# Optimization experiments

Hardware: AMD Instinct MI355X
Metric: run time of the kernel (lower is better)

The kernel has to match this reference:

```python
import jax, jax.numpy as jnp
import numpy as np

N_NODES = 50000
N_EDGES = 800000
D = 128          # embed_dim
H = 8            # heads
C = D // H       # per-head channels
F = 512          # ff_hidden_dim
LN_EPS = 1e-5
NEG_SLOPE = 0.2  # PyG GATConv default negative_slope


def _layernorm(x, g, b):
    mu = jnp.mean(x, axis=-1, keepdims=True)
    var = jnp.mean(jnp.square(x - mu), axis=-1, keepdims=True)
    return (x - mu) * jax.lax.rsqrt(var + LN_EPS) * g + b


def _gat_conv(x, edge_index, W, att_src, att_dst, bias):
    # PyG GATConv (concat=True, add_self_loops=True, shared lin for src/dst)
    N = x.shape[0]
    xl = (x @ W.T).reshape(N, H, C)                 # [N,H,C]
    a_s = jnp.sum(xl * att_src, axis=-1)            # [N,H]
    a_d = jnp.sum(xl * att_dst, axis=-1)            # [N,H]
    loops = jnp.arange(N)
    src = jnp.concatenate([edge_index[0], loops])   # [E+N]
    dst = jnp.concatenate([edge_index[1], loops])
    e = jax.nn.leaky_relu(a_s[src] + a_d[dst], NEG_SLOPE)  # [E+N,H]
    # segment softmax over incoming edges per destination node
    m = jax.ops.segment_max(e, dst, num_segments=N)
    m = jnp.where(jnp.isfinite(m), m, jnp.zeros_like(m))
    ex = jnp.exp(e - m[dst])
    s = jax.ops.segment_sum(ex, dst, num_segments=N)
    alpha = ex / (s[dst] + 1e-16)                   # [E+N,H]
    msg = xl[src] * alpha[:, :, None]               # [E+N,H,C]
    out = jax.ops.segment_sum(msg, dst, num_segments=N)  # [N,H,C]
    return out.reshape(N, H * C) + bias


def setup_inputs() -> dict:
    key = jax.random.key(0)
    ks = jax.random.split(key, 12)
    sc_d = 1.0 / np.sqrt(D)
    sc_f = 1.0 / np.sqrt(F)
    return {
        "x": jax.random.normal(ks[0], (N_NODES, D), dtype=jnp.float32),
        "virtual_edge_index": jax.random.randint(ks[1], (2, N_EDGES), 0, N_NODES, dtype=jnp.int64),
        "W_gat": jax.random.normal(ks[2], (H * C, D), dtype=jnp.float32) * sc_d,
        "att_src": jax.random.normal(ks[3], (H, C), dtype=jnp.float32) * sc_d,
        "att_dst": jax.random.normal(ks[4], (H, C), dtype=jnp.float32) * sc_d,
        "bias_gat": jnp.zeros((H * C,), dtype=jnp.float32),
        "W1": jax.random.normal(ks[5], (F, D), dtype=jnp.float32) * sc_d,
        "b1": jnp.zeros((F,), dtype=jnp.float32),
        "W2": jax.random.normal(ks[6], (D, F), dtype=jnp.float32) * sc_f,
        "b2": jnp.zeros((D,), dtype=jnp.float32),
        "g1": jnp.ones((D,), dtype=jnp.float32),
        "beta1": jnp.zeros((D,), dtype=jnp.float32),
        "g2": jnp.ones((D,), dtype=jnp.float32),
        "beta2": jnp.zeros((D,), dtype=jnp.float32),
    }


def reference(x, virtual_edge_index, W_gat, att_src, att_dst, bias_gat,
              W1, b1, W2, b2, g1, beta1, g2, beta2):
    h_gat = _gat_conv(x, virtual_edge_index, W_gat, att_src, att_dst, bias_gat)
    h = _layernorm(x + h_gat, g1, beta1)
    h_ff = jax.nn.relu(h @ W1.T + b1) @ W2.T + b2
    return _layernorm(h + h_ff, g2, beta2)
```

## Files before the change

kernel.cpp:

```cpp
#include <hip/hip_runtime.h>
#include <hip/hip_bf16.h>

#define N_NODES 50000
#define N_EDGES 800000
#define N_TOT   850000
#define DIM 128
#define HEADS 8
#define CH 16
#define FF 512
#define LN_EPS 1e-5f
#define NEG_SLOPE 0.2f

#define PART    8
#define NCHUNK  128
#define CHUNK_E (N_EDGES / NCHUNK)
#define NPP     (N_NODES / PART)
#define NHIST   (PART * NCHUNK)
#define NTILE   196

typedef __bf16 bf16x8 __attribute__((ext_vector_type(8)));
typedef float f32x4 __attribute__((ext_vector_type(4)));

__device__ __forceinline__ float bfr2f(unsigned short u) {
  return __uint_as_float(((unsigned)u) << 16);
}
__device__ __forceinline__ unsigned short f2bfr(float f) {
  __hip_bfloat16 h = __float2bfloat16(f);
  return *(unsigned short*)&h;
}
__device__ __forceinline__ float bf2f(__hip_bfloat16 h) { return __bfloat162float(h); }
__device__ __forceinline__ __hip_bfloat16 f2bf(float f) { return __float2bfloat16(f); }

__device__ __forceinline__ bf16x8 ldcvt8(const float* __restrict__ p) {
  const float4 a = ((const float4*)p)[0];
  const float4 b = ((const float4*)p)[1];
  bf16x8 r;
  r[0] = (__bf16)a.x; r[1] = (__bf16)a.y; r[2] = (__bf16)a.z; r[3] = (__bf16)a.w;
  r[4] = (__bf16)b.x; r[5] = (__bf16)b.y; r[6] = (__bf16)b.z; r[7] = (__bf16)b.w;
  return r;
}

__device__ __forceinline__ int ld_src(const int* ei, int mode, int e) {
  int v = mode ? ei[2 * e] : ei[e];
  return min(max(v, 0), N_NODES - 1);
}
__device__ __forceinline__ int ld_dst(const int* ei, int mode, int e) {
  int v = mode ? ei[2 * (N_EDGES + e)] : ei[N_EDGES + e];
  return min(max(v, 0), N_NODES - 1);
}
__device__ __forceinline__ int edge_mode(const int* __restrict__ ei) {
  int any = 0;
  for (int k = 1; k < 64; k += 2) any |= ei[k];
  return (any == 0) ? 1 : 0;
}

__device__ __forceinline__ float expleaky(float v) {
  v = v > 0.f ? v : NEG_SLOPE * v;
  return __expf(v);
}

__global__ __launch_bounds__(256) void k_xl(const float* __restrict__ x,
                                            const float* __restrict__ Wg,
                                            const float* __restrict__ att_s,
                                            const float* __restrict__ att_d,
                                            __hip_bfloat16* __restrict__ xl,
                                            float* __restrict__ a_s,
                                            float* __restrict__ a_d) {
  int gid = blockIdx.x * 256 + threadIdx.x;
  int w = gid >> 6;
  if (w >= 3125 * 2) return;
  int l = threadIdx.x & 63, quad = l >> 4, r = l & 15;
  int strip = w >> 1, cc = w & 1;
  f32x4 acc[4];
#pragma unroll
  for (int t = 0; t < 4; ++t) acc[t] = (f32x4){0.f, 0.f, 0.f, 0.f};
  int arow = strip * 16 + r;
  bf16x8 af[4];
#pragma unroll
  for (int kk = 0; kk < 4; ++kk) af[kk] = ldcvt8(x + arow * DIM + kk * 32 + quad * 8);
#pragma unroll
  for (int kk = 0; kk < 4; ++kk) {
    bf16x8 bfr[4];
#pragma unroll
    for (int t = 0; t < 4; ++t)
      bfr[t] = ldcvt8(Wg + (cc * 64 + t * 16 + r) * DIM + kk * 32 + quad * 8);
#pragma unroll
    for (int t = 0; t < 4; ++t)
      acc[t] = __builtin_amdgcn_mfma_f32_16x16x32_bf16(af[kk], bfr[t], acc[t], 0, 0, 0);
  }
  float ats[4], atd[4];
#pragma unroll
  for (int t = 0; t < 4; ++t) {
    ats[t] = att_s[(cc * 4 + t) * CH + r];
    atd[t] = att_d[(cc * 4 + t) * CH + r];
  }
#pragma unroll
  for (int t = 0; t < 4; ++t)
#pragma unroll
    for (int j = 0; j < 4; ++j) {
      int row = strip * 16 + quad * 4 + j;
      int col = cc * 64 + t * 16 + r;
      xl[row * DIM + col] = f2bf(acc[t][j]);
      float vs = acc[t][j] * ats[t];
      float vd = acc[t][j] * atd[t];
      vs += __shfl_xor(vs, 1); vd += __shfl_xor(vd, 1);
      vs += __shfl_xor(vs, 2); vd += __shfl_xor(vd, 2);
      vs += __shfl_xor(vs, 4); vd += __shfl_xor(vd, 4);
      vs += __shfl_xor(vs, 8); vd += __shfl_xor(vd, 8);
      if (r == 0) {
        a_s[row * 8 + cc * 4 + t] = vs;
        a_d[row * 8 + cc * 4 + t] = vd;
      }
    }
}

__global__ __launch_bounds__(256) void k_hist2(const int* __restrict__ ei,
                                               const float* __restrict__ W1,
                                               const float* __restrict__ W2,
                                               __hip_bfloat16* __restrict__ wb,
                                               unsigned short* __restrict__ blkh) {
  __shared__ unsigned int hist[NPP];
  int p = blockIdx.x & 7, c = blockIdx.x >> 3;
  int tid = threadIdx.x;
  int gi = blockIdx.x * 256 + tid;
  if (gi < 65536)        wb[gi] = f2bf(W1[gi]);
  else if (gi < 131072)  wb[gi] = f2bf(W2[gi - 65536]);
  for (int i = tid; i < NPP; i += 256) hist[i] = 0;
  int m = edge_mode(ei);
  __syncthreads();
  int nlo = p * NPP;
  int e1 = (c + 1) * CHUNK_E;
  for (int e = c * CHUNK_E + tid; e < e1; e += 256) {
    int d = ld_dst(ei, m, e) - nlo;
    if ((unsigned)d < (unsigned)NPP) atomicAdd(&hist[d], 1u);
  }
  __syncthreads();
  unsigned short* dst = blkh + (size_t)c * N_NODES + nlo;
  for (int i = tid; i < NPP; i += 256) dst[i] = (unsigned short)hist[i];
}

__global__ __launch_bounds__(1024) void k_nscan2(unsigned short* __restrict__ blkh,
                                                 int* __restrict__ deg,
                                                 int* __restrict__ tsum) {
  __shared__ int gs[4][256];
  __shared__ int red[4];
  int tid = threadIdx.x;
  int nl = tid & 255, g = tid >> 8;
  int n = blockIdx.x * 256 + nl;
  unsigned short vv[32];
  int gsum = 0;
  if (n < N_NODES) {
    const unsigned short* base = blkh + (size_t)(g * 32) * N_NODES + n;
#pragma unroll
    for (int i = 0; i < 32; ++i) {
      vv[i] = base[(size_t)i * N_NODES];
      gsum += (int)vv[i];
    }
  }
  gs[g][nl] = gsum;
  __syncthreads();
  int gexcl = 0;
#pragma unroll
  for (int j = 0; j < 4; ++j) if (j < g) gexcl += gs[j][nl];
  int total = gs[0][nl] + gs[1][nl] + gs[2][nl] + gs[3][nl];
  if (n < N_NODES) {
    unsigned short* base = blkh + (size_t)(g * 32) * N_NODES + n;
    int run = gexcl;
#pragma unroll
    for (int i = 0; i < 32; ++i) {
      int t = (int)vv[i];
      base[(size_t)i * N_NODES] = (unsigned short)run;
      run += t;
    }
    if (g == 0) deg[n] = total;
  }
  if (g == 0) {
    int val = (n < N_NODES) ? total + 1 : 0;
    int l = tid & 63, wv = tid >> 6;
#pragma unroll
    for (int off = 1; off < 64; off <<= 1) val += __shfl_xor(val, off);
    if (l == 0) red[wv] = val;
  }
  __syncthreads();
  if (tid == 0) tsum[blockIdx.x] = red[0] + red[1] + red[2] + red[3];
}

__global__ __launch_bounds__(256) void k_offs2(const int* __restrict__ deg,
                                               const int* __restrict__ tsum,
                                               int* __restrict__ offs,
                                               int* __restrict__ eid) {
  __shared__ int wtot[4];
  __shared__ int red[4];
  __shared__ int sbase;
  int tid = threadIdx.x, l = tid & 63, wv = tid >> 6;
  int bid = blockIdx.x;
  int part = (tid < bid) ? tsum[tid] : 0;
#pragma unroll
  for (int off = 1; off < 64; off <<= 1) part += __shfl_xor(part, off);
  if (l == 0) red[wv] = part;
  __syncthreads();
  if (tid == 0) sbase = (red[0] + red[1]) + (red[2] + red[3]);
  __syncthreads();
  int tbase = sbase;
  int n = bid * 256 + tid;
  int v = (n < N_NODES) ? deg[n] + 1 : 0;
  int xx = v;
#pragma unroll
  for (int off = 1; off < 64; off <<= 1) {
    int t = __shfl_up(xx, off);
    if (l >= off) xx += t;
  }
  if (l == 63) wtot[wv] = xx;
  __syncthreads();
  int wbase = 0;
#pragma unroll
  for (int j = 0; j < 4; ++j) if (j < wv) wbase += wtot[j];
  int excl = tbase + wbase + xx - v;
  if (n < N_NODES) {
    offs[n] = excl;
    eid[excl] = n;
    if (n == N_NODES - 1) offs[N_NODES] = excl + v;
  }
}

__global__ __launch_bounds__(256) void k_scatter(const int* __restrict__ ei,
                                                 const int* __restrict__ offs,
                                                 const unsigned short* __restrict__ blkh,
                                                 int* __restrict__ eid) {
  __shared__ unsigned int fill[NPP];
  int p = blockIdx.x & 7, c = blockIdx.x >> 3;
  int tid = threadIdx.x;
  for (int i = tid; i < NPP; i += 256) fill[i] = 0;
  int m = edge_mode(ei);
  __syncthreads();
  int nlo = p * NPP;
  const unsigned short* exl = blkh + (size_t)c * N_NODES;
  int e1 = (c + 1) * CHUNK_E;
  for (int e = c * CHUNK_E + tid; e < e1; e += 256) {
    int dg = ld_dst(ei, m, e);
    int d = dg - nlo;
    if ((unsigned)d < (unsigned)NPP) {
      unsigned ord = atomicAdd(&fill[d], 1u);
      int slot = offs[dg] + 1 + (int)exl[dg] + (int)ord;
      eid[slot] = ld_src(ei, m, e);
    }
  }
}

__global__ __launch_bounds__(256) void k_attn(const int* __restrict__ eid, const int* __restrict__ offs,
                                              const float* __restrict__ a_s,
                                              const float* __restrict__ a_d,
                                              const __hip_bfloat16* __restrict__ xl,
                                              const float* __restrict__ x,
                                              const float* __restrict__ bias,
                                              const float* __restrict__ g1,
                                              const float* __restrict__ be1,
                                              __hip_bfloat16* __restrict__ h1out) {
  int wv = threadIdx.x >> 6, l = threadIdx.x & 63;
  int n = blockIdx.x * 4 + wv;
  int start = offs[n], end = offs[n + 1];
  int h8 = l & 7, sl8 = l >> 3;
  int hq = l >> 3;
  float adv = a_d[n * 8 + h8];

  const char* xlb = (const char*)xl;
  int l4 = 4 * l;
  float sme = 0.f;
  float A0 = 0.f, A1 = 0.f;
  int p = start;
  int pend = start + ((end - start) & ~7);
  if (p < pend) {
    int s_nx = eid[p + sl8];
    float as_nx = a_s[s_nx * 8 + h8];
    while (p < pend) {
      int boff = s_nx << 8;
      float w = expleaky(as_nx + adv);
      p += 8;
      if (p < pend) {
        s_nx = eid[p + sl8];
        as_nx = a_s[s_nx * 8 + h8];
      }
      sme += w;
#pragma unroll
      for (int q = 0; q < 8; ++q) {
        int bq = __shfl(boff, q * 8);
        float wq = __shfl(w, q * 8 + hq);
        ushort2 u = *(const ushort2*)(xlb + bq + l4);
        A0 += wq * bfr2f(u.x);
        A1 += wq * bfr2f(u.y);
      }
    }
  }
  int rem = end - p;
  if (rem > 0) {
    int sl = (sl8 < rem) ? sl8 : 0;
    int s = eid[p + sl];
    int boff = s << 8;
    float w = (sl8 < rem) ? expleaky(a_s[s * 8 + h8] + adv) : 0.f;
    sme += w;
    for (int q = 0; q < rem; ++q) {
      int bq = __shfl(boff, q * 8);
      float wq = __shfl(w, q * 8 + hq);
      ushort2 u = *(const ushort2*)(xlb + bq + l4);
      A0 += wq * bfr2f(u.x);
      A1 += wq * bfr2f(u.y);
    }
  }
  sme += __shfl_xor(sme, 8);
  sme += __shfl_xor(sme, 16);
  sme += __shfl_xor(sme, 32);
  float smh = __shfl(sme, hq);
  float inv = 1.f / (smh + 1e-16f);
  float acc0 = A0 * inv;
  float acc1 = A1 * inv;

  float2 xv = *(const float2*)(x + n * DIM + 2 * l);
  float2 bv = *(const float2*)(bias + 2 * l);
  float v0 = acc0 + bv.x + xv.x;
  float v1 = acc1 + bv.y + xv.y;
  float s2 = v0 + v1;
  for (int off = 32; off >= 1; off >>= 1) s2 += __shfl_xor(s2, off);
  float mu = s2 * (1.f / 128.f);
  float d0 = v0 - mu, d1 = v1 - mu;
  float q = d0 * d0 + d1 * d1;
  for (int off = 32; off >= 1; off >>= 1) q += __shfl_xor(q, off);
  float rs = rsqrtf(q * (1.f / 128.f) + LN_EPS);
  float2 gv = *(const float2*)(g1 + 2 * l);
  float2 bev = *(const float2*)(be1 + 2 * l);
  ushort2 o;
  o.x = f2bfr(d0 * rs * gv.x + bev.x);
  o.y = f2bfr(d1 * rs * gv.y + bev.y);
  *(ushort2*)((unsigned short*)h1out + n * DIM + 2 * l) = o;
}

__global__ __launch_bounds__(256) void k_ffn1(const __hip_bfloat16* __restrict__ h1,
                                              const __hip_bfloat16* __restrict__ W1b,
                                              const float* __restrict__ b1,
                                              __hip_bfloat16* __restrict__ hid,
                                              int row_base) {
  int wv = threadIdx.x >> 6, l = threadIdx.x & 63, quad = l >> 4, r = l & 15;
  int blk = blockIdx.x;
  int base = row_base + blk * 32;
  const __bf16* h1b = (const __bf16*)h1;
  const __bf16* w1 = (const __bf16*)W1b;
  int r0 = min(base + r, N_NODES - 1);
  int r1 = min(base + 16 + r, N_NODES - 1);

  bf16x8 bn[2][4];
#pragma unroll
  for (int kk = 0; kk < 4; ++kk) {
    bn[0][kk] = *(const bf16x8*)(h1b + r0 * DIM + kk * 32 + quad * 8);
    bn[1][kk] = *(const bf16x8*)(h1b + r1 * DIM + kk * 32 + quad * 8);
  }
  f32x4 acc1[8][2];
#pragma unroll
  for (int tm = 0; tm < 8; ++tm)
#pragma unroll
    for (int tn = 0; tn < 2; ++tn) acc1[tm][tn] = (f32x4){0.f, 0.f, 0.f, 0.f};
#pragma unroll
  for (int kk = 0; kk < 4; ++kk) {
    bf16x8 wf[8];
#pragma unroll
    for (int tm = 0; tm < 8; ++tm)
      wf[tm] = *(const bf16x8*)(w1 + (wv * 128 + tm * 16 + r) * DIM + kk * 32 + quad * 8);
#pragma unroll
    for (int tm = 0; tm < 8; ++tm) {
      acc1[tm][0] = __builtin_amdgcn_mfma_f32_16x16x32_bf16(wf[tm], bn[0][kk], acc1[tm][0], 0, 0, 0);
      acc1[tm][1] = __builtin_amdgcn_mfma_f32_16x16x32_bf16(wf[tm], bn[1][kk], acc1[tm][1], 0, 0, 0);
    }
  }
  unsigned short* hb = (unsigned short*)hid;
#pragma unroll
  for (int tm = 0; tm < 8; ++tm) {
    int f0 = wv * 128 + tm * 16 + quad * 4;
    float4 bb = *(const float4*)(b1 + f0);
#pragma unroll
    for (int tn = 0; tn < 2; ++tn) {
      ushort4 o;
      o.x = f2bfr(fmaxf(acc1[tm][tn][0] + bb.x, 0.f));
      o.y = f2bfr(fmaxf(acc1[tm][tn][1] + bb.y, 0.f));
      o.z = f2bfr(fmaxf(acc1[tm][tn][2] + bb.z, 0.f));
      o.w = f2bfr(fmaxf(acc1[tm][tn][3] + bb.w, 0.f));
      int idx = ((blk * 2 + tn) * 64 + wv * 16 + tm * 2 + (quad >> 1)) * 128
                + r * 8 + (quad & 1) * 4;
      *(ushort4*)(hb + idx) = o;
    }
  }
}

__global__ __launch_bounds__(256) void k_ffn2(const __hip_bfloat16* __restrict__ hid,
                                              const __hip_bfloat16* __restrict__ W2b,
                                              const float* __restrict__ b2,
                                              const float* __restrict__ g2,
                                              const float* __restrict__ be2,
                                              const __hip_bfloat16* __restrict__ h1,
                                              float* __restrict__ out,
                                              int row_base) {
  __shared__ float ps[4][2][16], pq[4][2][16];
  int wv = threadIdx.x >> 6, l = threadIdx.x & 63, quad = l >> 4, r = l & 15;
  int blk = blockIdx.x;
  int base = row_base + blk * 32;
  const __bf16* w2 = (const __bf16*)W2b;
  const unsigned short* hb = (const unsigned short*)hid;

  f32x4 acc2[2][2];
#pragma unroll
  for (int s = 0; s < 2; ++s)
#pragma unroll
    for (int tn = 0; tn < 2; ++tn) acc2[s][tn] = (f32x4){0.f, 0.f, 0.f, 0.f};

  const unsigned short* a0base = hb + ((blk * 2 + 0) * 64 + quad) * 128 + r * 8;
  const unsigned short* a1base = hb + ((blk * 2 + 1) * 64 + quad) * 128 + r * 8;
  const __bf16* w2base = w2 + (wv * 32 + r) * FF + quad * 8;

#pragma unroll 4
  for (int ka = 0; ka < 16; ++ka) {
    bf16x8 a0 = *(const bf16x8*)(a0base + ka * 512);
    bf16x8 a1 = *(const bf16x8*)(a1base + ka * 512);
    bf16x8 wa0 = *(const bf16x8*)(w2base + ka * 32);
    bf16x8 wa1 = *(const bf16x8*)(w2base + 16 * FF + ka * 32);
    acc2[0][0] = __builtin_amdgcn_mfma_f32_16x16x32_bf16(a0, wa0, acc2[0][0], 0, 0, 0);
    acc2[0][1] = __builtin_amdgcn_mfma_f32_16x16x32_bf16(a0, wa1, acc2[0][1], 0, 0, 0);
    acc2[1][0] = __builtin_amdgcn_mfma_f32_16x16x32_bf16(a1, wa0, acc2[1][0], 0, 0, 0);
    acc2[1][1] = __builtin_amdgcn_mfma_f32_16x16x32_bf16(a1, wa1, acc2[1][1], 0, 0, 0);
  }
#pragma unroll
  for (int s = 0; s < 2; ++s)
#pragma unroll
    for (int tn = 0; tn < 2; ++tn) {
      int col = wv * 32 + tn * 16 + r;
      float b2c = b2[col];
#pragma unroll
      for (int j = 0; j < 4; ++j) {
        int row = min(base + s * 16 + quad * 4 + j, N_NODES - 1);
        acc2[s][tn][j] += b2c + bf2f(h1[row * DIM + col]);
      }
    }
#pragma unroll
  for (int s = 0; s < 2; ++s)
#pragma unroll
    for (int j = 0; j < 4; ++j) {
      float sm = acc2[s][0][j] + acc2[s][1][j];
      float qm = acc2[s][0][j] * acc2[s][0][j] + acc2[s][1][j] * acc2[s][1][j];
      sm += __shfl_xor(sm, 1); sm += __shfl_xor(sm, 2); sm += __shfl_xor(sm, 4); sm += __shfl_xor(sm, 8);
      qm += __shfl_xor(qm, 1); qm += __shfl_xor(qm, 2); qm += __shfl_xor(qm, 4); qm += __shfl_xor(qm, 8);
      if (r == j) { ps[wv][s][quad * 4 + j] = sm; pq[wv][s][quad * 4 + j] = qm; }
    }
  __syncthreads();
#pragma unroll
  for (int s = 0; s < 2; ++s)
#pragma unroll
    for (int j = 0; j < 4; ++j) {
      int row16 = quad * 4 + j;
      float st = (ps[0][s][row16] + ps[1][s][row16]) + (ps[2][s][row16] + ps[3][s][row16]);
      float qt = (pq[0][s][row16] + pq[1][s][row16]) + (pq[2][s][row16] + pq[3][s][row16]);
      float mu = st * (1.f / 128.f);
      float var = qt * (1.f / 128.f) - mu * mu;
      float rs = rsqrtf(var + LN_EPS);
      int grow = base + s * 16 + row16;
      if (grow < N_NODES) {
#pragma unroll
        for (int tn = 0; tn < 2; ++tn) {
          int col = wv * 32 + tn * 16 + r;
          out[grow * DIM + col] = (acc2[s][tn][j] - mu) * rs * g2[col] + be2[col];
        }
      }
    }
}

#define OFF_H1     0u
#define SZ_H1      (50016u * DIM * 2u)
#define OFF_WB     (OFF_H1 + SZ_H1)
#define SZ_WB      262144u
#define OFF_XL     (OFF_WB + SZ_WB)
#define SZ_XL      (N_NODES * DIM * 2u)
#define OFF_AS     (OFF_XL + SZ_XL)
#define SZ_AS      (N_NODES * HEADS * 4u)
#define OFF_AD     (OFF_AS + SZ_AS)
#define OFF_DEG    (OFF_AD + SZ_AS)
#define SZ_DEG     200192u
#define OFF_OFFS   (OFF_DEG + SZ_DEG)
#define SZ_OFFS    200448u
#define OFF_EID    (OFF_OFFS + SZ_OFFS)
#define SZ_EID     3400192u
#define OFF_BLKH   (OFF_EID + SZ_EID)
#define SZ_BLKH    (NCHUNK * (unsigned)N_NODES * 2u)
#define OFF_TSUM   (OFF_BLKH + SZ_BLKH)
#define OFF_HID    OFF_XL
#define SZ_HID_FULL  (50016u * FF * 2u)
#define FFN_CHUNK0_BLOCKS 782
#define FFN_CHUNK1_BLOCKS 781
#define FFN_CHUNK0_ROWS   (FFN_CHUNK0_BLOCKS * 32)

extern "C" void kernel_launch(void* const* d_in, const int* in_sizes, int n_in,
                              void* d_out, int out_size, void* d_ws, size_t ws_size,
                              hipStream_t stream) {
  const float* x     = (const float*)d_in[0];
  const int*   ei    = (const int*)d_in[1];
  const float* Wg    = (const float*)d_in[2];
  const float* att_s = (const float*)d_in[3];
  const float* att_d = (const float*)d_in[4];
  const float* bias  = (const float*)d_in[5];
  const float* W1    = (const float*)d_in[6];
  const float* b1    = (const float*)d_in[7];
  const float* W2    = (const float*)d_in[8];
  const float* b2    = (const float*)d_in[9];
  const float* g1    = (const float*)d_in[10];
  const float* be1   = (const float*)d_in[11];
  const float* g2    = (const float*)d_in[12];
  const float* be2   = (const float*)d_in[13];

  char* ws = (char*)d_ws;
  __hip_bfloat16* h1     = (__hip_bfloat16*)(ws + OFF_H1);
  __hip_bfloat16* wbuf   = (__hip_bfloat16*)(ws + OFF_WB);
  __hip_bfloat16* W1b    = wbuf;
  __hip_bfloat16* W2b    = wbuf + 65536;
  __hip_bfloat16* xl     = (__hip_bfloat16*)(ws + OFF_XL);
  float*          a_s    = (float*)(ws + OFF_AS);
  float*          a_d    = (float*)(ws + OFF_AD);
  int*            deg    = (int*)(ws + OFF_DEG);
  int*            offs   = (int*)(ws + OFF_OFFS);
  int*            eid    = (int*)(ws + OFF_EID);
  unsigned short* blkh   = (unsigned short*)(ws + OFF_BLKH);
  int*            tsum   = (int*)(ws + OFF_TSUM);
  __hip_bfloat16* hid    = (__hip_bfloat16*)(ws + OFF_HID);
  float*          out    = (float*)d_out;

  k_xl     <<<1563,  256, 0, stream>>>(x, Wg, att_s, att_d, xl, a_s, a_d);
  k_hist2  <<<NHIST, 256, 0, stream>>>(ei, W1, W2, wbuf, blkh);
  k_nscan2 <<<NTILE, 1024, 0, stream>>>(blkh, deg, tsum);
  k_offs2  <<<NTILE,  256, 0, stream>>>(deg, tsum, offs, eid);
  k_scatter<<<NHIST,  256, 0, stream>>>(ei, offs, blkh, eid);
  k_attn   <<<12500,  256, 0, stream>>>(eid, offs, a_s, a_d, xl, x, bias, g1, be1, h1);
  if (ws_size >= (size_t)OFF_HID + SZ_HID_FULL) {
    k_ffn1 <<<1563, 256, 0, stream>>>(h1, W1b, b1, hid, 0);
    k_ffn2 <<<1563, 256, 0, stream>>>(hid, W2b, b2, g2, be2, h1, out, 0);
  } else {
    k_ffn1 <<<FFN_CHUNK0_BLOCKS, 256, 0, stream>>>(h1, W1b, b1, hid, 0);
    k_ffn2 <<<FFN_CHUNK0_BLOCKS, 256, 0, stream>>>(hid, W2b, b2, g2, be2, h1, out, 0);
    k_ffn1 <<<FFN_CHUNK1_BLOCKS, 256, 0, stream>>>(h1, W1b, b1, hid, FFN_CHUNK0_ROWS);
    k_ffn2 <<<FFN_CHUNK1_BLOCKS, 256, 0, stream>>>(hid, W2b, b2, g2, be2, h1, out, FFN_CHUNK0_ROWS);
  }
}
```

Baseline: 305.2 us.

## Pre-convert GAT weight to bf16, halve CSR partitions, simplify attention loop

```diff
diff --git a/kernel.cpp b/kernel.cpp
--- a/kernel.cpp
+++ b/kernel.cpp
@@ -11,11 +11,11 @@
 #define LN_EPS 1e-5f
 #define NEG_SLOPE 0.2f
 
-#define PART    8
+#define CSR_PART 4
 #define NCHUNK  128
 #define CHUNK_E (N_EDGES / NCHUNK)
-#define NPP     (N_NODES / PART)
-#define NHIST   (PART * NCHUNK)
+#define NPP     (N_NODES / CSR_PART)
+#define NHIST   (CSR_PART * NCHUNK)
 #define NTILE   196
 
 typedef __bf16 bf16x8 __attribute__((ext_vector_type(8)));
@@ -59,8 +59,35 @@
   return __expf(v);
 }
 
+__global__ __launch_bounds__(256) void k_hist2(const int* __restrict__ ei,
+                                               const float* __restrict__ Wg,
+                                               const float* __restrict__ W1,
+                                               const float* __restrict__ W2,
+                                               __hip_bfloat16* __restrict__ wb,
+                                               unsigned short* __restrict__ blkh) {
+  __shared__ unsigned int hist[NPP];
+  int p = blockIdx.x & 3, c = blockIdx.x >> 2;
+  int tid = threadIdx.x;
+  int gi = blockIdx.x * 256 + tid;
+  if (gi < 65536) wb[16384 + gi] = f2bf(W1[gi]);
+  else            wb[16384 + gi] = f2bf(W2[gi - 65536]);
+  if (gi < 16384) wb[gi] = f2bf(Wg[gi]);
+  for (int i = tid; i < NPP; i += 256) hist[i] = 0;
+  int m = edge_mode(ei);
+  __syncthreads();
+  int nlo = p * NPP;
+  int e1 = (c + 1) * CHUNK_E;
+  for (int e = c * CHUNK_E + tid; e < e1; e += 256) {
+    int d = ld_dst(ei, m, e) - nlo;
+    if ((unsigned)d < (unsigned)NPP) atomicAdd(&hist[d], 1u);
+  }
+  __syncthreads();
+  unsigned short* dst = blkh + (size_t)c * N_NODES + nlo;
+  for (int i = tid; i < NPP; i += 256) dst[i] = (unsigned short)hist[i];
+}
+
 __global__ __launch_bounds__(256) void k_xl(const float* __restrict__ x,
-                                            const float* __restrict__ Wg,
+                                            const __hip_bfloat16* __restrict__ Wgb,
                                             const float* __restrict__ att_s,
                                             const float* __restrict__ att_d,
                                             __hip_bfloat16* __restrict__ xl,
@@ -71,6 +98,7 @@
   if (w >= 3125 * 2) return;
   int l = threadIdx.x & 63, quad = l >> 4, r = l & 15;
   int strip = w >> 1, cc = w & 1;
+  const __bf16* wgb = (const __bf16*)Wgb;
   f32x4 acc[4];
 #pragma unroll
   for (int t = 0; t < 4; ++t) acc[t] = (f32x4){0.f, 0.f, 0.f, 0.f};
@@ -83,7 +111,7 @@
     bf16x8 bfr[4];
 #pragma unroll
     for (int t = 0; t < 4; ++t)
-      bfr[t] = ldcvt8(Wg + (cc * 64 + t * 16 + r) * DIM + kk * 32 + quad * 8);
+      bfr[t] = *(const bf16x8*)(wgb + (cc * 64 + t * 16 + r) * DIM + kk * 32 + quad * 8);
 #pragma unroll
     for (int t = 0; t < 4; ++t)
       acc[t] = __builtin_amdgcn_mfma_f32_16x16x32_bf16(af[kk], bfr[t], acc[t], 0, 0, 0);
@@ -114,31 +142,6 @@
     }
 }
 
-__global__ __launch_bounds__(256) void k_hist2(const int* __restrict__ ei,
-                                               const float* __restrict__ W1,
-                                               const float* __restrict__ W2,
-                                               __hip_bfloat16* __restrict__ wb,
-                                               unsigned short* __restrict__ blkh) {
-  __shared__ unsigned int hist[NPP];
-  int p = blockIdx.x & 7, c = blockIdx.x >> 3;
-  int tid = threadIdx.x;
-  int gi = blockIdx.x * 256 + tid;
-  if (gi < 65536)        wb[gi] = f2bf(W1[gi]);
-  else if (gi < 131072)  wb[gi] = f2bf(W2[gi - 65536]);
-  for (int i = tid; i < NPP; i += 256) hist[i] = 0;
-  int m = edge_mode(ei);
-  __syncthreads();
-  int nlo = p * NPP;
-  int e1 = (c + 1) * CHUNK_E;
-  for (int e = c * CHUNK_E + tid; e < e1; e += 256) {
-    int d = ld_dst(ei, m, e) - nlo;
-    if ((unsigned)d < (unsigned)NPP) atomicAdd(&hist[d], 1u);
-  }
-  __syncthreads();
-  unsigned short* dst = blkh + (size_t)c * N_NODES + nlo;
-  for (int i = tid; i < NPP; i += 256) dst[i] = (unsigned short)hist[i];
-}
-
 __global__ __launch_bounds__(1024) void k_nscan2(unsigned short* __restrict__ blkh,
                                                  int* __restrict__ deg,
                                                  int* __restrict__ tsum) {
@@ -228,7 +231,7 @@
                                                  const unsigned short* __restrict__ blkh,
                                                  int* __restrict__ eid) {
   __shared__ unsigned int fill[NPP];
-  int p = blockIdx.x & 7, c = blockIdx.x >> 3;
+  int p = blockIdx.x & 3, c = blockIdx.x >> 2;
   int tid = threadIdx.x;
   for (int i = tid; i < NPP; i += 256) fill[i] = 0;
   int m = edge_mode(ei);
@@ -268,27 +271,18 @@
   float sme = 0.f;
   float A0 = 0.f, A1 = 0.f;
   int p = start;
-  int pend = start + ((end - start) & ~7);
-  if (p < pend) {
-    int s_nx = eid[p + sl8];
-    float as_nx = a_s[s_nx * 8 + h8];
-    while (p < pend) {
-      int boff = s_nx << 8;
-      float w = expleaky(as_nx + adv);
-      p += 8;
-      if (p < pend) {
-        s_nx = eid[p + sl8];
-        as_nx = a_s[s_nx * 8 + h8];
-      }
-      sme += w;
-#pragma unroll
-      for (int q = 0; q < 8; ++q) {
-        int bq = __shfl(boff, q * 8);
-        float wq = __shfl(w, q * 8 + hq);
-        ushort2 u = *(const ushort2*)(xlb + bq + l4);
-        A0 += wq * bfr2f(u.x);
-        A1 += wq * bfr2f(u.y);
-      }
+  for (; p + 8 <= end; p += 8) {
+    int s = eid[p + sl8];
+    int boff = s << 8;
+    float w = expleaky(a_s[s * 8 + h8] + adv);
+    sme += w;
+#pragma unroll
+    for (int q = 0; q < 8; ++q) {
+      int bq = __shfl(boff, q * 8);
+      float wq = __shfl(w, q * 8 + hq);
+      ushort2 u = *(const ushort2*)(xlb + bq + l4);
+      A0 += wq * bfr2f(u.x);
+      A1 += wq * bfr2f(u.y);
     }
   }
   int rem = end - p;
@@ -471,7 +465,7 @@
 #define OFF_H1     0u
 #define SZ_H1      (50016u * DIM * 2u)
 #define OFF_WB     (OFF_H1 + SZ_H1)
-#define SZ_WB      262144u
+#define SZ_WB      294912u
 #define OFF_XL     (OFF_WB + SZ_WB)
 #define SZ_XL      (N_NODES * DIM * 2u)
 #define OFF_AS     (OFF_XL + SZ_XL)
@@ -513,8 +507,9 @@
   char* ws = (char*)d_ws;
   __hip_bfloat16* h1     = (__hip_bfloat16*)(ws + OFF_H1);
   __hip_bfloat16* wbuf   = (__hip_bfloat16*)(ws + OFF_WB);
-  __hip_bfloat16* W1b    = wbuf;
-  __hip_bfloat16* W2b    = wbuf + 65536;
+  __hip_bfloat16* Wgb    = wbuf;
+  __hip_bfloat16* W1b    = wbuf + 16384;
+  __hip_bfloat16* W2b    = wbuf + 81920;
   __hip_bfloat16* xl     = (__hip_bfloat16*)(ws + OFF_XL);
   float*          a_s    = (float*)(ws + OFF_AS);
   float*          a_d    = (float*)(ws + OFF_AD);
@@ -526,8 +521,8 @@
   __hip_bfloat16* hid    = (__hip_bfloat16*)(ws + OFF_HID);
   float*          out    = (float*)d_out;
 
-  k_xl     <<<1563,  256, 0, stream>>>(x, Wg, att_s, att_d, xl, a_s, a_d);
-  k_hist2  <<<NHIST, 256, 0, stream>>>(ei, W1, W2, wbuf, blkh);
+  k_hist2  <<<NHIST,  256, 0, stream>>>(ei, Wg, W1, W2, wbuf, blkh);
+  k_xl     <<<1563,   256, 0, stream>>>(x, Wgb, att_s, att_d, xl, a_s, a_d);
   k_nscan2 <<<NTILE, 1024, 0, stream>>>(blkh, deg, tsum);
   k_offs2  <<<NTILE,  256, 0, stream>>>(deg, tsum, offs, eid);
   k_scatter<<<NHIST,  256, 0, stream>>>(ei, offs, blkh, eid);
```

New measurement: 291.1 us (median of 2 runs). 1.05x faster.
